# Optimization experiments

Hardware: AMD Instinct MI355X
Metric: run time of the kernel (lower is better)

Reference implementation:

```python
import jax, jax.numpy as jnp
import numpy as np

SEQ = 4096
EMB = 1024
OUT = 1024


def setup_inputs() -> dict:
    key = jax.random.key(0)
    k_x, k_q, k_k, k_v = jax.random.split(key, 4)
    scale = 1.0 / np.sqrt(EMB)
    inputs = jax.random.normal(k_x, (SEQ, EMB), dtype=jnp.float32)
    # torch Linear weight is (out_features, in_features); y = x @ W.T
    W_Q = jax.random.normal(k_q, (OUT, EMB), dtype=jnp.float32) * scale
    W_K = jax.random.normal(k_k, (OUT, EMB), dtype=jnp.float32) * scale
    W_V = jax.random.normal(k_v, (OUT, EMB), dtype=jnp.float32) * scale
    return {"inputs": inputs, "W_Q": W_Q, "W_K": W_K, "W_V": W_V}


def reference(inputs, W_Q, W_K, W_V):
    # projections: (S, E) @ (E, D) -> (S, D)
    q = inputs @ W_Q.T
    k = inputs @ W_K.T
    v = inputs @ W_V.T
    d_k = k.shape[-1]
    scores = (q @ k.T) / jnp.sqrt(jnp.asarray(d_k, dtype=q.dtype))  # (S, S)
    weights = jax.nn.softmax(scores, axis=-1)
    return weights @ v  # (S, D)
```

## Files before the change

kernel.cpp:

```cpp
#include <hip/hip_runtime.h>

typedef __bf16 bf16;
typedef __bf16 bf16x4 __attribute__((ext_vector_type(4)));
typedef __bf16 bf16x8 __attribute__((ext_vector_type(8)));
typedef float f32x4 __attribute__((ext_vector_type(4)));

#define SEQ 4096
#define EMB 1024

__device__ __forceinline__ void async_copy16(void* lds, const void* g) {
    __builtin_amdgcn_global_load_lds(
        (const __attribute__((address_space(1))) unsigned int*)g,
        (__attribute__((address_space(3))) unsigned int*)lds,
        16, 0, 0);
}

__global__ __launch_bounds__(256) void prep_all(const float* __restrict__ x,
                                                const float* __restrict__ wq,
                                                const float* __restrict__ wk,
                                                const float* __restrict__ wv,
                                                bf16* __restrict__ xb,
                                                bf16* __restrict__ wqk,
                                                bf16* __restrict__ wvb,
                                                float* __restrict__ rowsum)
{
    const int u = blockIdx.x * 256 + threadIdx.x;
    const float* src;
    bf16* dst;
    int off;
    if (u < 1048576)      { src = x;  dst = xb;               off = u; }
    else if (u < 1310720) { src = wq; dst = wqk;              off = u - 1048576; }
    else if (u < 1572864) { src = wk; dst = wqk + EMB * EMB;  off = u - 1310720; }
    else if (u < 1835008) { src = wv; dst = wvb;              off = u - 1572864; }
    else {
        *(float4*)(rowsum + (size_t)(u - 1835008) * 4) = float4{0.f, 0.f, 0.f, 0.f};
        return;
    }
    float4 f = *(const float4*)(src + (size_t)off * 4);
    bf16x4 v = { (bf16)f.x, (bf16)f.y, (bf16)f.z, (bf16)f.w };
    *(bf16x4*)(dst + (size_t)off * 4) = v;
}

template<bool RSUM>
__device__ __forceinline__ void gemm_core(const bf16* __restrict__ A,
                                          const bf16* __restrict__ B,
                                          int lda, int ldb, int K, long koff,
                                          int m0, int n0,
                                          bf16* __restrict__ As, bf16* __restrict__ Bs,
                                          f32x4 (&acc)[4][4], float (&rsum)[4],
                                          bool rs_active)
{
    const int tid  = threadIdx.x;
    const int lane = tid & 63;
    const int wave = tid >> 6;
    const int srow = tid >> 3;
    const int spc  = tid & 7;
    const int sl   = (spc - (srow & 7)) & 7;
    const int wm = (wave & 1) << 6;
    const int wn = (wave >> 1) << 6;
    const int fr = lane & 15;
    const int q  = lane >> 4;

    for (int i = 0; i < 4; i++)
        for (int j = 0; j < 4; j++)
            acc[i][j] = {0.f, 0.f, 0.f, 0.f};
    if (RSUM)
        for (int i = 0; i < 4; i++) rsum[i] = 0.f;

    const bf16* Ab = A + (size_t)(m0 + srow) * lda + koff + sl * 8;
    const bf16* Bb = B + (size_t)(n0 + srow) * ldb + koff + sl * 8;
    bf16* AsD = &As[srow * 64 + spc * 8];
    bf16* BsD = &Bs[srow * 64 + spc * 8];

    const int pc0 = ((q + fr) & 7) * 8;
    const int pc1 = pc0 ^ 32;

    for (int k0 = 0; k0 < K; k0 += 64) {
        __syncthreads();
        for (int t = 0; t < 4; t++) {
            async_copy16(AsD + t * 2048, Ab + k0 + (size_t)(32 * t) * lda);
            async_copy16(BsD + t * 2048, Bb + k0 + (size_t)(32 * t) * ldb);
        }
        __syncthreads();

        bf16x8 af[4], bg[4];
        for (int i = 0; i < 4; i++)
            af[i] = *(const bf16x8*)&As[(wm + i * 16 + fr) * 64 + pc0];
        for (int j = 0; j < 4; j++)
            bg[j] = *(const bf16x8*)&Bs[(wn + j * 16 + fr) * 64 + pc0];
        if (RSUM && rs_active)
            for (int i = 0; i < 4; i++)
                for (int e = 0; e < 8; e++) rsum[i] += (float)af[i][e];
        for (int i = 0; i < 4; i++)
            for (int j = 0; j < 4; j++)
                acc[i][j] = __builtin_amdgcn_mfma_f32_16x16x32_bf16(af[i], bg[j], acc[i][j], 0, 0, 0);

        for (int i = 0; i < 4; i++)
            af[i] = *(const bf16x8*)&As[(wm + i * 16 + fr) * 64 + pc1];
        for (int j = 0; j < 4; j++)
            bg[j] = *(const bf16x8*)&Bs[(wn + j * 16 + fr) * 64 + pc1];
        if (RSUM && rs_active)
            for (int i = 0; i < 4; i++)
                for (int e = 0; e < 8; e++) rsum[i] += (float)af[i][e];
        for (int i = 0; i < 4; i++)
            for (int j = 0; j < 4; j++)
                acc[i][j] = __builtin_amdgcn_mfma_f32_16x16x32_bf16(af[i], bg[j], acc[i][j], 0, 0, 0);
    }
}

__global__ __launch_bounds__(256) void gemm_proj(const bf16* __restrict__ xb,
                                                 const bf16* __restrict__ wqk,
                                                 const bf16* __restrict__ wvb,
                                                 bf16* __restrict__ QK,
                                                 bf16* __restrict__ VT)
{
    __shared__ __align__(16) bf16 As[128 * 64];
    __shared__ __align__(16) bf16 Bs[128 * 64];

    const bf16 *A, *B;
    bf16* C;
    int ldc, m0, n0;
    if (blockIdx.y < 16) {
        A = xb; B = wqk; C = QK; ldc = 2048;
        m0 = blockIdx.x * 128; n0 = blockIdx.y * 128;
    } else {
        A = wvb; B = xb; C = VT; ldc = 4096;
        m0 = (blockIdx.x & 7) * 128;
        n0 = ((blockIdx.x >> 3) + ((blockIdx.y - 16) << 2)) * 128;
    }

    f32x4 acc[4][4];
    float rs[4];
    gemm_core<false>(A, B, 1024, 1024, 1024, 0, m0, n0, As, Bs, acc, rs, false);

    const int lane = threadIdx.x & 63;
    const int wave = threadIdx.x >> 6;
    const int cm = m0 + ((wave & 1) << 6) + ((lane >> 4) << 2);
    const int cn = n0 + ((wave >> 1) << 6) + (lane & 15);
    for (int i = 0; i < 4; i++)
        for (int j = 0; j < 4; j++)
            for (int r = 0; r < 4; r++)
                C[(size_t)(cm + i * 16 + r) * ldc + (cn + j * 16)] = (bf16)acc[i][j][r];
}

__global__ __launch_bounds__(256) void gemm_exp(const bf16* __restrict__ QK,
                                                bf16* __restrict__ E)
{
    __shared__ __align__(16) bf16 As[128 * 64];
    __shared__ __align__(16) bf16 Bs[128 * 64];

    const int m0 = blockIdx.x * 128;
    const int n0 = blockIdx.y * 128;
    f32x4 acc[4][4];
    float rs[4];
    gemm_core<false>(QK, QK + 1024, 2048, 2048, 1024, 0, m0, n0, As, Bs, acc, rs, false);

    const int lane = threadIdx.x & 63;
    const int wave = threadIdx.x >> 6;
    const int cm = m0 + ((wave & 1) << 6) + ((lane >> 4) << 2);
    const int cn = n0 + ((wave >> 1) << 6) + (lane & 15);
    for (int i = 0; i < 4; i++)
        for (int j = 0; j < 4; j++)
            for (int r = 0; r < 4; r++)
                E[(size_t)(cm + i * 16 + r) * 4096 + (cn + j * 16)] =
                    (bf16)__expf(acc[i][j][r] * 0.03125f);
}

__global__ __launch_bounds__(256) void gemm_pv(const bf16* __restrict__ E,
                                               const bf16* __restrict__ VT,
                                               float* __restrict__ out,
                                               float* __restrict__ p1,
                                               float* __restrict__ rowsum)
{
    __shared__ __align__(16) bf16 As[128 * 64];
    __shared__ __align__(16) bf16 Bs[128 * 64];

    const int m0 = blockIdx.x * 128;
    const int n0 = blockIdx.y * 128;
    const long koff = (long)blockIdx.z * 1024;
    const bool rs_active = (blockIdx.y == 0) && (threadIdx.x < 128);

    f32x4 acc[4][4];
    float rs[4];
    gemm_core<true>(E, VT, 4096, 4096, 1024, koff, m0, n0, As, Bs, acc, rs, rs_active);

    const int lane = threadIdx.x & 63;
    const int wave = threadIdx.x >> 6;
    if (rs_active) {
        for (int i = 0; i < 4; i++) {
            rs[i] += __shfl_xor(rs[i], 16);
            rs[i] += __shfl_xor(rs[i], 32);
        }
        if (lane < 16) {
            const int wm = (wave & 1) << 6;
            for (int i = 0; i < 4; i++)
                unsafeAtomicAdd(&rowsum[m0 + wm + i * 16 + lane], rs[i]);
        }
    }

    float* C = (blockIdx.z == 0) ? out : p1 + (size_t)(blockIdx.z - 1) * SEQ * 1024;
    const int cm = m0 + ((wave & 1) << 6) + ((lane >> 4) << 2);
    const int cn = n0 + ((wave >> 1) << 6) + (lane & 15);
    for (int i = 0; i < 4; i++)
        for (int j = 0; j < 4; j++)
            for (int r = 0; r < 4; r++)
                C[(size_t)(cm + i * 16 + r) * 1024 + (cn + j * 16)] = acc[i][j][r];
}

__global__ __launch_bounds__(256) void reduce_norm(float* __restrict__ out,
                                                   const float* __restrict__ p1,
                                                   const float* __restrict__ p2,
                                                   const float* __restrict__ p3,
                                                   const float* __restrict__ rowsum)
{
    const int m = blockIdx.x;
    const float inv = 1.f / rowsum[m];
    const size_t off = (size_t)m * 1024 + threadIdx.x * 4;
    float4 a = *(const float4*)(out + off);
    float4 b = *(const float4*)(p1 + off);
    float4 c = *(const float4*)(p2 + off);
    float4 d = *(const float4*)(p3 + off);
    float4 o;
    o.x = (a.x + b.x + c.x + d.x) * inv;
    o.y = (a.y + b.y + c.y + d.y) * inv;
    o.z = (a.z + b.z + c.z + d.z) * inv;
    o.w = (a.w + b.w + c.w + d.w) * inv;
    *(float4*)(out + off) = o;
}

extern "C" void kernel_launch(void* const* d_in, const int* in_sizes, int n_in,
                              void* d_out, int out_size, void* d_ws, size_t ws_size,
                              hipStream_t stream)
{
    const float* x  = (const float*)d_in[0];
    const float* wq = (const float*)d_in[1];
    const float* wk = (const float*)d_in[2];
    const float* wv = (const float*)d_in[3];
    float* out = (float*)d_out;

    char* ws = (char*)d_ws;
    const size_t MB = 1024 * 1024;
    bf16*  E   = (bf16*)(ws);
    float* p1  = (float*)(ws + 32 * MB);
    float* p2  = (float*)(ws + 48 * MB);
    float* p3  = (float*)(ws + 64 * MB);
    bf16*  xb  = (bf16*)(ws + 32 * MB);
    bf16*  wqk = (bf16*)(ws + 40 * MB);
    bf16*  wvb = (bf16*)(ws + 44 * MB);
    bf16*  QK  = (bf16*)(ws + 64 * MB);
    bf16*  VT  = (bf16*)(ws + 80 * MB);
    float* rsm = (float*)(ws + 88 * MB);

    dim3 blk(256);

    prep_all<<<dim3(7172), blk, 0, stream>>>(x, wq, wk, wv, xb, wqk, wvb, rsm);
    gemm_proj<<<dim3(32, 24), blk, 0, stream>>>(xb, wqk, wvb, QK, VT);
    gemm_exp<<<dim3(32, 32), blk, 0, stream>>>(QK, E);
    gemm_pv<<<dim3(32, 8, 4), blk, 0, stream>>>(E, VT, out, p1, rsm);
    reduce_norm<<<dim3(4096), blk, 0, stream>>>(out, p1, p2, p3, rsm);
}
```

Measured before the change: 215.9 us.

## Fuse all attention stages into one persistent kernel with grid barriers

Replaces the five separate launches (convert, projection GEMM, exp-score GEMM, PV GEMM, reduce/normalize) with a single persistent kernel of 512 blocks. The blocks step through each phase in grid-stride loops and synchronize between phases with atomic-counter grid barriers, which removes inter-kernel launch gaps and tail drains. The split-K partial outputs of the PV GEMM are now stored as bf16 instead of fp32, halving partial-sum traffic at some cost in accuracy. The barriers assume all 512 blocks are co-resident (two per CU), otherwise the kernel deadlocks, and the fixed grid can load-balance unevenly in phases whose job counts are not multiples of 512.

```diff
diff --git a/kernel.cpp b/kernel.cpp
--- a/kernel.cpp
+++ b/kernel.cpp
@@ -7,6 +7,7 @@
 
 #define SEQ 4096
 #define EMB 1024
+#define NBLK 512
 
 __device__ __forceinline__ void async_copy16(void* lds, const void* g) {
     __builtin_amdgcn_global_load_lds(
@@ -15,30 +16,16 @@
         16, 0, 0);
 }
 
-__global__ __launch_bounds__(256) void prep_all(const float* __restrict__ x,
-                                                const float* __restrict__ wq,
-                                                const float* __restrict__ wk,
-                                                const float* __restrict__ wv,
-                                                bf16* __restrict__ xb,
-                                                bf16* __restrict__ wqk,
-                                                bf16* __restrict__ wvb,
-                                                float* __restrict__ rowsum)
-{
-    const int u = blockIdx.x * 256 + threadIdx.x;
-    const float* src;
-    bf16* dst;
-    int off;
-    if (u < 1048576)      { src = x;  dst = xb;               off = u; }
-    else if (u < 1310720) { src = wq; dst = wqk;              off = u - 1048576; }
-    else if (u < 1572864) { src = wk; dst = wqk + EMB * EMB;  off = u - 1310720; }
-    else if (u < 1835008) { src = wv; dst = wvb;              off = u - 1572864; }
-    else {
-        *(float4*)(rowsum + (size_t)(u - 1835008) * 4) = float4{0.f, 0.f, 0.f, 0.f};
-        return;
-    }
-    float4 f = *(const float4*)(src + (size_t)off * 4);
-    bf16x4 v = { (bf16)f.x, (bf16)f.y, (bf16)f.z, (bf16)f.w };
-    *(bf16x4*)(dst + (size_t)off * 4) = v;
+__device__ __forceinline__ void grid_barrier(unsigned* cnt) {
+    __syncthreads();
+    __threadfence();
+    if (threadIdx.x == 0) {
+        __hip_atomic_fetch_add(cnt, 1u, __ATOMIC_ACQ_REL, __HIP_MEMORY_SCOPE_AGENT);
+        while (__hip_atomic_load(cnt, __ATOMIC_ACQUIRE, __HIP_MEMORY_SCOPE_AGENT) < NBLK)
+            __builtin_amdgcn_s_sleep(32);
+    }
+    __syncthreads();
+    __threadfence();
 }
 
 template<bool RSUM>
@@ -108,124 +95,115 @@
     }
 }
 
-__global__ __launch_bounds__(256) void gemm_proj(const bf16* __restrict__ xb,
-                                                 const bf16* __restrict__ wqk,
-                                                 const bf16* __restrict__ wvb,
-                                                 bf16* __restrict__ QK,
-                                                 bf16* __restrict__ VT)
+__global__ __launch_bounds__(256, 2) void attention_all(
+    const float* __restrict__ x,  const float* __restrict__ wq,
+    const float* __restrict__ wk, const float* __restrict__ wv,
+    bf16* __restrict__ xb, bf16* __restrict__ wqk, bf16* __restrict__ wvb,
+    bf16* __restrict__ QK, bf16* __restrict__ VT, bf16* __restrict__ E,
+    bf16* __restrict__ pb,
+    float* __restrict__ rsm, float* __restrict__ out,
+    unsigned* __restrict__ bar)
 {
     __shared__ __align__(16) bf16 As[128 * 64];
     __shared__ __align__(16) bf16 Bs[128 * 64];
 
-    const bf16 *A, *B;
-    bf16* C;
-    int ldc, m0, n0;
-    if (blockIdx.y < 16) {
-        A = xb; B = wqk; C = QK; ldc = 2048;
-        m0 = blockIdx.x * 128; n0 = blockIdx.y * 128;
-    } else {
-        A = wvb; B = xb; C = VT; ldc = 4096;
-        m0 = (blockIdx.x & 7) * 128;
-        n0 = ((blockIdx.x >> 3) + ((blockIdx.y - 16) << 2)) * 128;
-    }
+    const int bid  = blockIdx.x;
+    const int tid  = threadIdx.x;
+    const int lane = tid & 63;
+    const int wave = tid >> 6;
+    const int cmo = ((wave & 1) << 6) + ((lane >> 4) << 2);
+    const int cno = ((wave >> 1) << 6) + (lane & 15);
 
     f32x4 acc[4][4];
     float rs[4];
-    gemm_core<false>(A, B, 1024, 1024, 1024, 0, m0, n0, As, Bs, acc, rs, false);
-
-    const int lane = threadIdx.x & 63;
-    const int wave = threadIdx.x >> 6;
-    const int cm = m0 + ((wave & 1) << 6) + ((lane >> 4) << 2);
-    const int cn = n0 + ((wave >> 1) << 6) + (lane & 15);
-    for (int i = 0; i < 4; i++)
-        for (int j = 0; j < 4; j++)
-            for (int r = 0; r < 4; r++)
-                C[(size_t)(cm + i * 16 + r) * ldc + (cn + j * 16)] = (bf16)acc[i][j][r];
-}
-
-__global__ __launch_bounds__(256) void gemm_exp(const bf16* __restrict__ QK,
-                                                bf16* __restrict__ E)
-{
-    __shared__ __align__(16) bf16 As[128 * 64];
-    __shared__ __align__(16) bf16 Bs[128 * 64];
-
-    const int m0 = blockIdx.x * 128;
-    const int n0 = blockIdx.y * 128;
-    f32x4 acc[4][4];
-    float rs[4];
-    gemm_core<false>(QK, QK + 1024, 2048, 2048, 1024, 0, m0, n0, As, Bs, acc, rs, false);
-
-    const int lane = threadIdx.x & 63;
-    const int wave = threadIdx.x >> 6;
-    const int cm = m0 + ((wave & 1) << 6) + ((lane >> 4) << 2);
-    const int cn = n0 + ((wave >> 1) << 6) + (lane & 15);
-    for (int i = 0; i < 4; i++)
-        for (int j = 0; j < 4; j++)
-            for (int r = 0; r < 4; r++)
-                E[(size_t)(cm + i * 16 + r) * 4096 + (cn + j * 16)] =
-                    (bf16)__expf(acc[i][j][r] * 0.03125f);
-}
-
-__global__ __launch_bounds__(256) void gemm_pv(const bf16* __restrict__ E,
-                                               const bf16* __restrict__ VT,
-                                               float* __restrict__ out,
-                                               float* __restrict__ p1,
-                                               float* __restrict__ rowsum)
-{
-    __shared__ __align__(16) bf16 As[128 * 64];
-    __shared__ __align__(16) bf16 Bs[128 * 64];
-
-    const int m0 = blockIdx.x * 128;
-    const int n0 = blockIdx.y * 128;
-    const long koff = (long)blockIdx.z * 1024;
-    const bool rs_active = (blockIdx.y == 0) && (threadIdx.x < 128);
-
-    f32x4 acc[4][4];
-    float rs[4];
-    gemm_core<true>(E, VT, 4096, 4096, 1024, koff, m0, n0, As, Bs, acc, rs, rs_active);
-
-    const int lane = threadIdx.x & 63;
-    const int wave = threadIdx.x >> 6;
-    if (rs_active) {
-        for (int i = 0; i < 4; i++) {
-            rs[i] += __shfl_xor(rs[i], 16);
-            rs[i] += __shfl_xor(rs[i], 32);
-        }
-        if (lane < 16) {
-            const int wm = (wave & 1) << 6;
-            for (int i = 0; i < 4; i++)
-                unsafeAtomicAdd(&rowsum[m0 + wm + i * 16 + lane], rs[i]);
-        }
-    }
-
-    float* C = (blockIdx.z == 0) ? out : p1 + (size_t)(blockIdx.z - 1) * SEQ * 1024;
-    const int cm = m0 + ((wave & 1) << 6) + ((lane >> 4) << 2);
-    const int cn = n0 + ((wave >> 1) << 6) + (lane & 15);
-    for (int i = 0; i < 4; i++)
-        for (int j = 0; j < 4; j++)
-            for (int r = 0; r < 4; r++)
-                C[(size_t)(cm + i * 16 + r) * 1024 + (cn + j * 16)] = acc[i][j][r];
-}
-
-__global__ __launch_bounds__(256) void reduce_norm(float* __restrict__ out,
-                                                   const float* __restrict__ p1,
-                                                   const float* __restrict__ p2,
-                                                   const float* __restrict__ p3,
-                                                   const float* __restrict__ rowsum)
-{
-    const int m = blockIdx.x;
-    const float inv = 1.f / rowsum[m];
-    const size_t off = (size_t)m * 1024 + threadIdx.x * 4;
-    float4 a = *(const float4*)(out + off);
-    float4 b = *(const float4*)(p1 + off);
-    float4 c = *(const float4*)(p2 + off);
-    float4 d = *(const float4*)(p3 + off);
-    float4 o;
-    o.x = (a.x + b.x + c.x + d.x) * inv;
-    o.y = (a.y + b.y + c.y + d.y) * inv;
-    o.z = (a.z + b.z + c.z + d.z) * inv;
-    o.w = (a.w + b.w + c.w + d.w) * inv;
-    *(float4*)(out + off) = o;
+
+    for (int u = bid * 256 + tid; u < 1836032; u += NBLK * 256) {
+        const float* src; bf16* dst; int off;
+        if (u < 1048576)      { src = x;  dst = xb;              off = u; }
+        else if (u < 1310720) { src = wq; dst = wqk;             off = u - 1048576; }
+        else if (u < 1572864) { src = wk; dst = wqk + EMB * EMB; off = u - 1310720; }
+        else if (u < 1835008) { src = wv; dst = wvb;             off = u - 1572864; }
+        else {
+            *(float4*)(rsm + (size_t)(u - 1835008) * 4) = float4{0.f, 0.f, 0.f, 0.f};
+            continue;
+        }
+        float4 f = *(const float4*)(src + (size_t)off * 4);
+        bf16x4 v = { (bf16)f.x, (bf16)f.y, (bf16)f.z, (bf16)f.w };
+        *(bf16x4*)(dst + (size_t)off * 4) = v;
+    }
+    grid_barrier(bar + 0);
+
+    for (int j = bid; j < 768; j += NBLK) {
+        const bf16 *A, *B; bf16* C; int ldc, m0, n0;
+        if (j < 512) {
+            A = xb; B = wqk; C = QK; ldc = 2048;
+            m0 = (j & 31) * 128; n0 = (j >> 5) * 128;
+        } else {
+            const int jj = j - 512;
+            A = wvb; B = xb; C = VT; ldc = 4096;
+            m0 = (jj & 7) * 128;
+            n0 = (((jj & 31) >> 3) + (jj >> 5) * 4) * 128;
+        }
+        gemm_core<false>(A, B, 1024, 1024, 1024, 0, m0, n0, As, Bs, acc, rs, false);
+        const int cm = m0 + cmo, cn = n0 + cno;
+        for (int i = 0; i < 4; i++)
+            for (int jx = 0; jx < 4; jx++)
+                for (int r = 0; r < 4; r++)
+                    C[(size_t)(cm + i * 16 + r) * ldc + (cn + jx * 16)] = (bf16)acc[i][jx][r];
+    }
+    grid_barrier(bar + 1);
+
+    for (int j = bid; j < 1024; j += NBLK) {
+        const int m0 = (j & 31) * 128, n0 = (j >> 5) * 128;
+        gemm_core<false>(QK, QK + 1024, 2048, 2048, 1024, 0, m0, n0, As, Bs, acc, rs, false);
+        const int cm = m0 + cmo, cn = n0 + cno;
+        for (int i = 0; i < 4; i++)
+            for (int jx = 0; jx < 4; jx++)
+                for (int r = 0; r < 4; r++)
+                    E[(size_t)(cm + i * 16 + r) * 4096 + (cn + jx * 16)] =
+                        (bf16)__expf(acc[i][jx][r] * 0.03125f);
+    }
+    grid_barrier(bar + 2);
+
+    for (int j = bid; j < 1024; j += NBLK) {
+        const int m0 = (j & 31) * 128, n0 = ((j >> 5) & 7) * 128, z = j >> 8;
+        const bool rs_active = (n0 == 0) && (tid < 128);
+        gemm_core<true>(E, VT, 4096, 4096, 1024, (long)z * 1024, m0, n0,
+                        As, Bs, acc, rs, rs_active);
+        if (rs_active) {
+            for (int i = 0; i < 4; i++) {
+                rs[i] += __shfl_xor(rs[i], 16);
+                rs[i] += __shfl_xor(rs[i], 32);
+            }
+            if (lane < 16) {
+                const int wm = (wave & 1) << 6;
+                for (int i = 0; i < 4; i++)
+                    unsafeAtomicAdd(&rsm[m0 + wm + i * 16 + lane], rs[i]);
+            }
+        }
+        bf16* C = pb + (size_t)z * SEQ * 1024;
+        const int cm = m0 + cmo, cn = n0 + cno;
+        for (int i = 0; i < 4; i++)
+            for (int jx = 0; jx < 4; jx++)
+                for (int r = 0; r < 4; r++)
+                    C[(size_t)(cm + i * 16 + r) * 1024 + (cn + jx * 16)] = (bf16)acc[i][jx][r];
+    }
+    grid_barrier(bar + 3);
+
+    for (int m = bid; m < 4096; m += NBLK) {
+        const float inv = 1.f / rsm[m];
+        const size_t off = (size_t)m * 1024 + tid * 4;
+        bf16x4 a = *(const bf16x4*)(pb + off);
+        bf16x4 b = *(const bf16x4*)(pb + (size_t)SEQ * 1024 + off);
+        bf16x4 c = *(const bf16x4*)(pb + (size_t)2 * SEQ * 1024 + off);
+        bf16x4 d = *(const bf16x4*)(pb + (size_t)3 * SEQ * 1024 + off);
+        float4 o;
+        o.x = ((float)a[0] + (float)b[0] + (float)c[0] + (float)d[0]) * inv;
+        o.y = ((float)a[1] + (float)b[1] + (float)c[1] + (float)d[1]) * inv;
+        o.z = ((float)a[2] + (float)b[2] + (float)c[2] + (float)d[2]) * inv;
+        o.w = ((float)a[3] + (float)b[3] + (float)c[3] + (float)d[3]) * inv;
+        *(float4*)(out + off) = o;
+    }
 }
 
 extern "C" void kernel_launch(void* const* d_in, const int* in_sizes, int n_in,
@@ -241,21 +219,17 @@
     char* ws = (char*)d_ws;
     const size_t MB = 1024 * 1024;
     bf16*  E   = (bf16*)(ws);
-    float* p1  = (float*)(ws + 32 * MB);
-    float* p2  = (float*)(ws + 48 * MB);
-    float* p3  = (float*)(ws + 64 * MB);
+    bf16*  pb  = (bf16*)(ws + 32 * MB);
     bf16*  xb  = (bf16*)(ws + 32 * MB);
     bf16*  wqk = (bf16*)(ws + 40 * MB);
     bf16*  wvb = (bf16*)(ws + 44 * MB);
     bf16*  QK  = (bf16*)(ws + 64 * MB);
     bf16*  VT  = (bf16*)(ws + 80 * MB);
     float* rsm = (float*)(ws + 88 * MB);
-
-    dim3 blk(256);
-
-    prep_all<<<dim3(7172), blk, 0, stream>>>(x, wq, wk, wv, xb, wqk, wvb, rsm);
-    gemm_proj<<<dim3(32, 24), blk, 0, stream>>>(xb, wqk, wvb, QK, VT);
-    gemm_exp<<<dim3(32, 32), blk, 0, stream>>>(QK, E);
-    gemm_pv<<<dim3(32, 8, 4), blk, 0, stream>>>(E, VT, out, p1, rsm);
-    reduce_norm<<<dim3(4096), blk, 0, stream>>>(out, p1, p2, p3, rsm);
-}
+    unsigned* bar = (unsigned*)(ws + 88 * MB + 16384);
+
+    hipMemsetAsync(bar, 0, 64, stream);
+
+    attention_all<<<dim3(NBLK), dim3(256), 0, stream>>>(
+        x, wq, wk, wv, xb, wqk, wvb, QK, VT, E, pb, rsm, out, bar);
+}
```

After: 822.3 us. 281% more time.
